# Kernel tuning notes

Hardware: AMD Instinct MI355X
Metric: run time of the kernel (lower is better)

The kernel has to match this reference:

```python
import jax, jax.numpy as jnp
import numpy as np

DEPTH = 3  # truncation depth of the signature


def setup_inputs() -> dict:
    key = jax.random.key(0)
    # (batch, stream, channels)
    path = jax.random.normal(key, (512, 512, 8), dtype=jnp.float32)
    return {"path": path}


def _signature(path, depth):
    """Truncated path signature via Chen's identity scanned over increments.

    Signature = exp(dx_1) (x) exp(dx_2) (x) ... truncated at `depth`, scalar
    level dropped; levels are kept flattened as (B, C**k) and concatenated
    at the end (flatten=True, stream=False, basepoint=False).
    """
    B, L, C = path.shape
    inc = path[:, 1:, :] - path[:, :-1, :]  # (B, L-1, C) path increments

    def exp_terms(dx):
        # truncated tensor exponential of a single increment: e_j = dx^{(x)j} / j!
        e = [dx]
        for j in range(2, depth + 1):
            e.append(jnp.einsum('bi,bc->bic', e[-1], dx).reshape(B, -1) / j)
        return e

    def chen_step(sig, dx):
        # Chen: new_k = e_k + S_k + sum_{i=1..k-1} S_i (x) e_{k-i}
        e = exp_terms(dx)
        new = []
        for k in range(1, depth + 1):
            t = sig[k - 1] + e[k - 1]
            for i in range(1, k):
                t = t + jnp.einsum('bi,bj->bij', sig[i - 1], e[k - i - 1]).reshape(B, -1)
            new.append(t)
        return tuple(new), None

    # zero init acts as the empty signature (only scalar level 1 implicit)
    init = tuple(jnp.zeros((B, C ** k), dtype=path.dtype) for k in range(1, depth + 1))
    sig, _ = jax.lax.scan(chen_step, init, jnp.swapaxes(inc, 0, 1))  # scan over stream
    return jnp.concatenate(sig, axis=-1)  # (B, C + C^2 + ... + C^depth)


def reference(path):
    return _signature(path, DEPTH)
```

## Files before the change

### kernel.cpp

```cpp
#include <hip/hip_runtime.h>

#define LSTREAM 512
#define C 8
#define OUTD 584
#define NW 16
#define SEG 32
#define INCF 4096
#define PSTRIDE 600

__device__ __forceinline__ void chen_combine(const float* bp, int i, int j, int lane,
                                             float& s1i, float& s2, float (&s3)[C]) {
    const float  b1i  = bp[i];
    const float  b1j  = bp[j];
    const float4 b1lo = *reinterpret_cast<const float4*>(bp);
    const float4 b1hi = *reinterpret_cast<const float4*>(bp + 4);
    const float4 b2lo = *reinterpret_cast<const float4*>(bp + C + j * C);
    const float4 b2hi = *reinterpret_cast<const float4*>(bp + C + j * C + 4);
    const float  b2ij = bp[C + lane];
    const float4 b3lo = *reinterpret_cast<const float4*>(bp + C + 64 + lane * C);
    const float4 b3hi = *reinterpret_cast<const float4*>(bp + C + 64 + lane * C + 4);
    const float b1k[C]  = {b1lo.x, b1lo.y, b1lo.z, b1lo.w, b1hi.x, b1hi.y, b1hi.z, b1hi.w};
    const float b2jk[C] = {b2lo.x, b2lo.y, b2lo.z, b2lo.w, b2hi.x, b2hi.y, b2hi.z, b2hi.w};
    const float b3k[C]  = {b3lo.x, b3lo.y, b3lo.z, b3lo.w, b3hi.x, b3hi.y, b3hi.z, b3hi.w};
    #pragma unroll
    for (int k = 0; k < C; ++k)
        s3[k] = s3[k] + b3k[k] + s1i * b2jk[k] + s2 * b1k[k];
    s2 = s2 + b2ij + s1i * b1j;
    s1i += b1i;
}

__device__ __forceinline__ void store_partial(float* pp, int i, int j, int lane,
                                              float s1i, float s2, const float (&s3)[C]) {
    if (j == 0) pp[i] = s1i;
    pp[C + lane] = s2;
    #pragma unroll
    for (int k = 0; k < C; ++k) pp[C + 64 + lane * C + k] = s3[k];
}

__global__ __launch_bounds__(1024, 8) void sig_kernel(const float* __restrict__ path,
                                                      float* __restrict__ out) {
    __shared__ float inc[INCF];
    __shared__ float part[NW * PSTRIDE];
    const int b    = blockIdx.x;
    const int tid  = threadIdx.x;
    const int w    = tid >> 6;
    const int lane = tid & 63;

    {
        const int row = tid >> 1;
        if (row < LSTREAM - 1) {
            const float4* p4 = reinterpret_cast<const float4*>(path + (size_t)b * (LSTREAM * C));
            const float4 a = p4[tid];
            const float4 c = p4[tid + 2];
            float4 d;
            d.x = c.x - a.x; d.y = c.y - a.y; d.z = c.z - a.z; d.w = c.w - a.w;
            reinterpret_cast<float4*>(inc)[tid] = d;
        }
    }
    __syncthreads();

    const int i = lane >> 3;
    const int j = lane & 7;

    float s1i = 0.f, s2 = 0.f;
    float s3[C];
    #pragma unroll
    for (int k = 0; k < C; ++k) s3[k] = 0.f;

    const int r0 = w * SEG;
    const int nst = min(SEG, (LSTREAM - 1) - r0);

    const float* ib = inc + r0 * C;
    #pragma unroll 4
    for (int t = 0; t < nst; ++t, ib += C) {
        const float4 a = *reinterpret_cast<const float4*>(ib);
        const float4 c = *reinterpret_cast<const float4*>(ib + 4);
        const float dx[C] = {a.x, a.y, a.z, a.w, c.x, c.y, c.z, c.w};
        const float dxi = ib[i];
        const float dxj = ib[j];

        const float u  = dxi * dxj;
        const float t1 = s1i * dxj;
        const float coeff = fmaf(u, (1.f / 6.f), fmaf(t1, 0.5f, s2));
        #pragma unroll
        for (int k = 0; k < C; ++k) s3[k] = fmaf(coeff, dx[k], s3[k]);
        s2 = fmaf(u, 0.5f, s2) + t1;
        s1i += dxi;
    }

    store_partial(part + w * PSTRIDE, i, j, lane, s1i, s2, s3);
    __syncthreads();

    if ((w & 1) == 0) chen_combine(part + (w + 1) * PSTRIDE, i, j, lane, s1i, s2, s3);
    if (w == 2 || w == 6 || w == 10 || w == 14)
        store_partial(part + w * PSTRIDE, i, j, lane, s1i, s2, s3);
    __syncthreads();

    if ((w & 3) == 0) chen_combine(part + (w + 2) * PSTRIDE, i, j, lane, s1i, s2, s3);
    if (w == 4 || w == 12)
        store_partial(part + w * PSTRIDE, i, j, lane, s1i, s2, s3);
    __syncthreads();

    if ((w & 7) == 0) chen_combine(part + (w + 4) * PSTRIDE, i, j, lane, s1i, s2, s3);
    if (w == 8)
        store_partial(part + w * PSTRIDE, i, j, lane, s1i, s2, s3);
    __syncthreads();

    if (w == 0) {
        chen_combine(part + 8 * PSTRIDE, i, j, lane, s1i, s2, s3);
        float* ob = out + (size_t)b * OUTD;
        const float s1out = __shfl(s1i, (lane << 3) & 63, 64);
        if (lane < C) ob[lane] = s1out;
        ob[C + lane] = s2;
        #pragma unroll
        for (int k = 0; k < C; ++k) ob[C + 64 + lane * C + k] = s3[k];
    }
}

extern "C" void kernel_launch(void* const* d_in, const int* in_sizes, int n_in,
                              void* d_out, int out_size, void* d_ws, size_t ws_size,
                              hipStream_t stream) {
    const float* path = (const float*)d_in[0];
    float* out = (float*)d_out;
    const int B = in_sizes[0] / (LSTREAM * C);
    sig_kernel<<<B, 1024, 0, stream>>>(path, out);
}
```

Before: 15.43 us.

## Stream path rows via scalar loads and split level-3 accumulation into two sums

```diff
diff --git a/kernel.cpp b/kernel.cpp
--- a/kernel.cpp
+++ b/kernel.cpp
@@ -5,8 +5,12 @@
 #define OUTD 584
 #define NW 16
 #define SEG 32
-#define INCF 4096
 #define PSTRIDE 600
+
+typedef __attribute__((ext_vector_type(8))) float f32x8;
+
+#define SLOAD(dst, ptr) asm volatile("s_load_dwordx8 %0, %1, 0x0" : "=&s"(dst) : "s"(ptr))
+#define SWAIT(x)        asm volatile("s_waitcnt lgkmcnt(0)" : "+s"(x))
 
 __device__ __forceinline__ void chen_combine(const float* bp, int i, int j, int lane,
                                              float& s1i, float& s2, float (&s3)[C]) {
@@ -39,74 +43,78 @@
 
 __global__ __launch_bounds__(1024, 8) void sig_kernel(const float* __restrict__ path,
                                                       float* __restrict__ out) {
-    __shared__ float inc[INCF];
     __shared__ float part[NW * PSTRIDE];
     const int b    = blockIdx.x;
     const int tid  = threadIdx.x;
-    const int w    = tid >> 6;
+    const int wu   = __builtin_amdgcn_readfirstlane(tid >> 6);
     const int lane = tid & 63;
-
-    {
-        const int row = tid >> 1;
-        if (row < LSTREAM - 1) {
-            const float4* p4 = reinterpret_cast<const float4*>(path + (size_t)b * (LSTREAM * C));
-            const float4 a = p4[tid];
-            const float4 c = p4[tid + 2];
-            float4 d;
-            d.x = c.x - a.x; d.y = c.y - a.y; d.z = c.z - a.z; d.w = c.w - a.w;
-            reinterpret_cast<float4*>(inc)[tid] = d;
-        }
-    }
-    __syncthreads();
-
     const int i = lane >> 3;
     const int j = lane & 7;
 
+    const float* pb = path + (size_t)b * (LSTREAM * C);
+    const int r0 = wu * SEG;
+
+    f32x8 rowNew, rowPre;
+    SLOAD(rowNew, pb + (size_t)r0 * C);
+    SWAIT(rowNew);
+    SLOAD(rowPre, pb + (size_t)(r0 + 1) * C);
+
+    float pi_prev = pb[r0 * C + i];
+    float pj_prev = pb[r0 * C + j];
+
     float s1i = 0.f, s2 = 0.f;
-    float s3[C];
+    f32x8 F = {0.f, 0.f, 0.f, 0.f, 0.f, 0.f, 0.f, 0.f};
+    f32x8 G = {0.f, 0.f, 0.f, 0.f, 0.f, 0.f, 0.f, 0.f};
+
     #pragma unroll
-    for (int k = 0; k < C; ++k) s3[k] = 0.f;
+    for (int s = 0; s < SEG; ++s) {
+        SWAIT(rowPre);
+        const f32x8 rowOld = rowNew;
+        rowNew = rowPre;
+        const int rNxt = min(r0 + s + 2, LSTREAM - 1);
+        SLOAD(rowPre, pb + (size_t)rNxt * C);
 
-    const int r0 = w * SEG;
-    const int nst = min(SEG, (LSTREAM - 1) - r0);
-
-    const float* ib = inc + r0 * C;
-    #pragma unroll 4
-    for (int t = 0; t < nst; ++t, ib += C) {
-        const float4 a = *reinterpret_cast<const float4*>(ib);
-        const float4 c = *reinterpret_cast<const float4*>(ib + 4);
-        const float dx[C] = {a.x, a.y, a.z, a.w, c.x, c.y, c.z, c.w};
-        const float dxi = ib[i];
-        const float dxj = ib[j];
+        const int rCur = min(r0 + s + 1, LSTREAM - 1);
+        const float pi_c = pb[rCur * C + i];
+        const float pj_c = pb[rCur * C + j];
+        const float dxi = pi_c - pi_prev; pi_prev = pi_c;
+        const float dxj = pj_c - pj_prev; pj_prev = pj_c;
 
         const float u  = dxi * dxj;
         const float t1 = s1i * dxj;
         const float coeff = fmaf(u, (1.f / 6.f), fmaf(t1, 0.5f, s2));
         #pragma unroll
-        for (int k = 0; k < C; ++k) s3[k] = fmaf(coeff, dx[k], s3[k]);
+        for (int k = 0; k < C; ++k) F[k] = fmaf(coeff, rowNew[k], F[k]);
+        #pragma unroll
+        for (int k = 0; k < C; ++k) G[k] = fmaf(coeff, rowOld[k], G[k]);
         s2 = fmaf(u, 0.5f, s2) + t1;
         s1i += dxi;
     }
+    SWAIT(rowPre);
 
-    store_partial(part + w * PSTRIDE, i, j, lane, s1i, s2, s3);
+    float s3[C];
+    #pragma unroll
+    for (int k = 0; k < C; ++k) s3[k] = F[k] - G[k];
+
+    store_partial(part + wu * PSTRIDE, i, j, lane, s1i, s2, s3);
     __syncthreads();
 
-    if ((w & 1) == 0) chen_combine(part + (w + 1) * PSTRIDE, i, j, lane, s1i, s2, s3);
-    if (w == 2 || w == 6 || w == 10 || w == 14)
-        store_partial(part + w * PSTRIDE, i, j, lane, s1i, s2, s3);
+    if ((wu & 1) == 0) chen_combine(part + (wu + 1) * PSTRIDE, i, j, lane, s1i, s2, s3);
+    if (wu == 2 || wu == 6 || wu == 10 || wu == 14)
+        store_partial(part + wu * PSTRIDE, i, j, lane, s1i, s2, s3);
     __syncthreads();
 
-    if ((w & 3) == 0) chen_combine(part + (w + 2) * PSTRIDE, i, j, lane, s1i, s2, s3);
-    if (w == 4 || w == 12)
-        store_partial(part + w * PSTRIDE, i, j, lane, s1i, s2, s3);
+    if ((wu & 3) == 0) chen_combine(part + (wu + 2) * PSTRIDE, i, j, lane, s1i, s2, s3);
+    if (wu == 4 || wu == 12)
+        store_partial(part + wu * PSTRIDE, i, j, lane, s1i, s2, s3);
     __syncthreads();
 
-    if ((w & 7) == 0) chen_combine(part + (w + 4) * PSTRIDE, i, j, lane, s1i, s2, s3);
-    if (w == 8)
-        store_partial(part + w * PSTRIDE, i, j, lane, s1i, s2, s3);
+    if ((wu & 7) == 0) chen_combine(part + (wu + 4) * PSTRIDE, i, j, lane, s1i, s2, s3);
+    if (wu == 8)
+        store_partial(part + wu * PSTRIDE, i, j, lane, s1i, s2, s3);
     __syncthreads();
 
-    if (w == 0) {
+    if (wu == 0) {
         chen_combine(part + 8 * PSTRIDE, i, j, lane, s1i, s2, s3);
         float* ob = out + (size_t)b * OUTD;
         const float s1out = __shfl(s1i, (lane << 3) & 63, 64);
```

New measurement: 53.53 us. +246.9%, slower.
